# Kernel optimization log

Hardware: AMD Instinct MI355X
Metric: run time of the kernel (lower is better)

The kernel has to match this reference:

```python
import jax, jax.numpy as jnp
import numpy as np

P, V, D = 1024, 49408, 512


def setup_inputs() -> dict:
    key = jax.random.key(0)
    k1, k2 = jax.random.split(key)
    prompt_embs = jax.random.normal(k1, (P, D), dtype=jnp.float32)
    clip_embs = jax.random.normal(k2, (V, D), dtype=jnp.float32)
    return {"prompt_embs": prompt_embs, "clip_embs": clip_embs}


def reference(prompt_embs, clip_embs):
    # torch.cdist(p=2): Euclidean distance matrix [P, V].
    # ||a-b||^2 = ||a||^2 + ||b||^2 - 2 a.b ; sqrt is monotone so argmin of
    # the (clamped) squared distance matches argmin of the true distance.
    a2 = jnp.sum(prompt_embs * prompt_embs, axis=-1, keepdims=True)   # [P,1]
    b2 = jnp.sum(clip_embs * clip_embs, axis=-1)                      # [V]
    ab = jnp.einsum("pd,vd->pv", prompt_embs, clip_embs)              # [P,V]
    d2 = jnp.maximum(a2 + b2[None, :] - 2.0 * ab, 0.0)                # [P,V]
    prompt_ids = jnp.argmin(d2, axis=1)                               # [P]
    new_embs = clip_embs[prompt_ids]                                  # [P,D] gather
    return new_embs, prompt_ids
```

## Files before the change

kernel.cpp:

```cpp
#include <hip/hip_runtime.h>
#include <stdint.h>

#define NP 1024
#define NV 49408
#define ND 512
#define NTILE 48

typedef __attribute__((ext_vector_type(8))) __bf16 bf16x8;
typedef __attribute__((ext_vector_type(4))) float f32x4;
typedef __attribute__((ext_vector_type(4))) int i32x4;

__device__ inline unsigned long long pack_sv(float s, unsigned v) {
  unsigned u = __float_as_uint(s);
  u = (u & 0x80000000u) ? ~u : (u | 0x80000000u);
  return ((unsigned long long)u << 32) | (unsigned long long)v;
}

__global__ __launch_bounds__(256) void pack_a_k(const float* __restrict__ src,
                                                __bf16* __restrict__ dst) {
  int lane = threadIdx.x & 63;
  int row = blockIdx.x * 4 + (threadIdx.x >> 6);
  const float* r = src + (size_t)row * ND + lane * 8;
  float4 x0 = *(const float4*)r;
  float4 x1 = *(const float4*)(r + 4);
  float xs[8] = {x0.x, x0.y, x0.z, x0.w, x1.x, x1.y, x1.z, x1.w};
  bf16x8 hi, lo;
#pragma unroll
  for (int j = 0; j < 8; ++j) {
    float x = xs[j];
    __bf16 h = (__bf16)x;
    hi[j] = h;
    lo[j] = (__bf16)(x - (float)h);
  }
  const int mb = row >> 4, rr = row & 15;
  const int tHi = lane >> 2, g = lane & 3;
  size_t cHi = (((size_t)tHi * 64) + mb) * 64 + g * 16 + rr;
  size_t cLo = (((size_t)(tHi + 16) * 64) + mb) * 64 + g * 16 + rr;
  *(bf16x8*)(dst + cHi * 8) = hi;
  *(bf16x8*)(dst + cLo * 8) = lo;
}

__global__ __launch_bounds__(256) void pack_b_k(const float* __restrict__ src,
                                                __bf16* __restrict__ dst,
                                                float* __restrict__ sumsq) {
  int lane = threadIdx.x & 63;
  int row = blockIdx.x * 4 + (threadIdx.x >> 6);
  const float* r = src + (size_t)row * ND + lane * 8;
  float4 x0 = *(const float4*)r;
  float4 x1 = *(const float4*)(r + 4);
  float xs[8] = {x0.x, x0.y, x0.z, x0.w, x1.x, x1.y, x1.z, x1.w};
  bf16x8 hi, lo;
  float ss = 0.f;
#pragma unroll
  for (int j = 0; j < 8; ++j) {
    float x = xs[j];
    ss += x * x;
    __bf16 h = (__bf16)x;
    hi[j] = h;
    lo[j] = (__bf16)(x - (float)h);
  }
  __bf16* drow = dst + (size_t)row * 1024 + lane * 8;
  *(bf16x8*)drow = hi;
  *(bf16x8*)(drow + 512) = lo;
#pragma unroll
  for (int m = 1; m < 64; m <<= 1) ss += __shfl_xor(ss, m);
  if (lane == 0) sumsq[row] = ss;
}


__device__ __attribute__((always_inline)) static inline
void gll16(const char* src, char* dst) {
  __builtin_amdgcn_global_load_lds(
      (const __attribute__((address_space(1))) void*)src,
      (__attribute__((address_space(3))) void*)dst, 16, 0, 0);
}

__device__ __attribute__((always_inline)) static inline
bf16x8 lds_read(unsigned addr) {
  i32x4 d;
  asm volatile("ds_read_b128 %0, %1" : "=v"(d) : "v"(addr));
  return __builtin_bit_cast(bf16x8, d);
}

#define FENCE asm volatile("" ::: "memory")

__device__ __attribute__((always_inline)) static inline
int bByte(int t) {
  int tt = (t < NTILE) ? t : t - NTILE;
  return (tt & 15) * 64 + (tt >= 32 ? 1024 : 0);
}

template <int J>
__device__ __attribute__((always_inline)) static inline
void phase_op(f32x4 (&acc)[4][4], bf16x8 (&aE)[4], bf16x8 (&aO)[4],
              const char* Ab, const int (&voffA)[4],
              const char* srcBt, char* stB, unsigned bRead, int p) {
  constexpr int R0 = 2 * J, R1 = 2 * J + 1;
  constexpr int S0 = (2 * J + 4) % 6, S1 = (2 * J + 5) % 6;
  const int kB0 = bByte(2 * p + 4), kB1 = bByte(2 * p + 5);
  const int kAE = ((2 * p + 2) & 31) * 65536;
  const int kAO = ((2 * p + 3) & 31) * 65536;
  gll16(srcBt + kB0, stB + S0 * 8192);
  gll16(srcBt + kB0 + 131072, stB + S0 * 8192 + 4096);
  gll16(srcBt + kB1, stB + S1 * 8192);
  gll16(srcBt + kB1 + 131072, stB + S1 * 8192 + 4096);
  bf16x8 b0[4], b1[4];
#pragma unroll
  for (int n = 0; n < 4; ++n) b0[n] = lds_read(bRead + R0 * 8192 + n * 1024);
#pragma unroll
  for (int n = 0; n < 4; ++n) b1[n] = lds_read(bRead + R1 * 8192 + n * 1024);
  asm volatile("s_waitcnt vmcnt(8) lgkmcnt(4)" ::: "memory");
  __builtin_amdgcn_sched_barrier(0);
  __builtin_amdgcn_s_setprio(1);
#pragma unroll
  for (int m = 0; m < 4; ++m)
#pragma unroll
    for (int n = 0; n < 4; ++n)
      acc[m][n] = __builtin_amdgcn_mfma_f32_16x16x32_bf16(aE[m], b0[n], acc[m][n], 0, 0, 0);
  __builtin_amdgcn_s_setprio(0);
#pragma unroll
  for (int m = 0; m < 4; ++m)
    aE[m] = *(const bf16x8*)(Ab + voffA[m] + kAE);
  asm volatile("s_waitcnt vmcnt(8) lgkmcnt(0)" ::: "memory");
  __builtin_amdgcn_sched_barrier(0);
  __builtin_amdgcn_s_setprio(1);
#pragma unroll
  for (int m = 0; m < 4; ++m)
#pragma unroll
    for (int n = 0; n < 4; ++n)
      acc[m][n] = __builtin_amdgcn_mfma_f32_16x16x32_bf16(aO[m], b1[n], acc[m][n], 0, 0, 0);
  __builtin_amdgcn_s_setprio(0);
#pragma unroll
  for (int m = 0; m < 4; ++m)
    aO[m] = *(const bf16x8*)(Ab + voffA[m] + kAO);
  FENCE;
  __builtin_amdgcn_s_barrier();
  FENCE;
}

__global__ __launch_bounds__(256, 3) void gemm_argmin_k(const __bf16* __restrict__ A,
                                                        const __bf16* __restrict__ B,
                                                        const float* __restrict__ b2,
                                                        unsigned long long* __restrict__ best) {
  __shared__ __align__(16) char lds[49152];
  const int tid = threadIdx.x;
  const int lane = tid & 63;
  const int wid = tid >> 6;
  const int wm = wid >> 1;
  const int wn = wid & 1;

  const int d = blockIdx.x;
  const int o = (d & 7) * 386 + (d >> 3);
  const int bm = (o & 7) * 128;
  const int bn = (o >> 3) * 128;

  const int r = lane & 15, g = lane >> 4;
  const int rh = r >> 1;
  const unsigned lds0 =
      (unsigned)(uintptr_t)(const __attribute__((address_space(3))) char*)(const char*)lds;
  const unsigned bRead = lds0 + wn * 4096 + rh * 128 + (r & 1) * 64 + (((g + rh) & 3) << 4);

  const char* Ab = (const char*)A;
  int voffA[4];
#pragma unroll
  for (int m = 0; m < 4; ++m)
    voffA[m] = ((bm >> 4) + wm * 4 + m) * 1024 + lane * 16;

  const int srow = 2 * (tid >> 3) + ((tid >> 2) & 1);
  const int sc16 = ((tid & 3) - (tid >> 3)) & 3;
  const char* srcBt = (const char*)B + (size_t)(bn + srow) * 2048 + sc16 * 16;
  char* stB = (char*)lds + tid * 16;

  f32x4 acc[4][4] = {};
  bf16x8 aE[4], aO[4];

  gll16(srcBt + bByte(0), stB + 0);
  gll16(srcBt + bByte(0) + 131072, stB + 4096);
  gll16(srcBt + bByte(1), stB + 8192);
  gll16(srcBt + bByte(1) + 131072, stB + 8192 + 4096);
  gll16(srcBt + bByte(2), stB + 16384);
  gll16(srcBt + bByte(2) + 131072, stB + 16384 + 4096);
  gll16(srcBt + bByte(3), stB + 24576);
  gll16(srcBt + bByte(3) + 131072, stB + 24576 + 4096);
#pragma unroll
  for (int m = 0; m < 4; ++m)
    aE[m] = *(const bf16x8*)(Ab + voffA[m]);
#pragma unroll
  for (int m = 0; m < 4; ++m)
    aO[m] = *(const bf16x8*)(Ab + voffA[m] + 65536);
  asm volatile("s_waitcnt vmcnt(12)" ::: "memory");
  FENCE;
  __builtin_amdgcn_s_barrier();
  FENCE;

#pragma unroll 1
  for (int it = 0; it < 8; ++it) {
    const int p0 = 3 * it;
    phase_op<0>(acc, aE, aO, Ab, voffA, srcBt, stB, bRead, p0 + 0);
    phase_op<1>(acc, aE, aO, Ab, voffA, srcBt, stB, bRead, p0 + 1);
    phase_op<2>(acc, aE, aO, Ab, voffA, srcBt, stB, bRead, p0 + 2);
  }

  float bb[4];
#pragma unroll
  for (int n = 0; n < 4; ++n) bb[n] = b2[bn + wn * 64 + n * 16 + r];
#pragma unroll
  for (int m = 0; m < 4; ++m) {
#pragma unroll
    for (int reg = 0; reg < 4; ++reg) {
      unsigned long long pk = ~0ull;
#pragma unroll
      for (int n = 0; n < 4; ++n) {
        float s = bb[n] - 2.0f * acc[m][n][reg];
        unsigned long long cand = pack_sv(s, (unsigned)(bn + wn * 64 + n * 16 + r));
        pk = (cand < pk) ? cand : pk;
      }
#pragma unroll
      for (int msk = 1; msk < 16; msk <<= 1) {
        unsigned long long o2 = __shfl_xor(pk, msk);
        pk = (o2 < pk) ? o2 : pk;
      }
      if (r == 0) atomicMin(&best[bm + wm * 64 + m * 16 + g * 4 + reg], pk);
    }
  }
}

__global__ __launch_bounds__(256) void naive_argmin_k(const float* __restrict__ A,
                                                      const float* __restrict__ B,
                                                      unsigned long long* __restrict__ best) {
  __shared__ float arow[ND];
  int p = blockIdx.y;
  unsigned v = blockIdx.x * 256 + threadIdx.x;
  for (int i = threadIdx.x; i < ND; i += 256) arow[i] = A[(size_t)p * ND + i];
  __syncthreads();
  const float4* br = (const float4*)(B + (size_t)v * ND);
  float s = 0.f;
#pragma unroll 4
  for (int i = 0; i < ND / 4; ++i) {
    float4 b = br[i];
    const float4 a = *(const float4*)&arow[i * 4];
    float d0 = a.x - b.x, d1 = a.y - b.y, d2 = a.z - b.z, d3 = a.w - b.w;
    s += d0 * d0 + d1 * d1 + d2 * d2 + d3 * d3;
  }
  unsigned long long pk = pack_sv(s, v);
#pragma unroll
  for (int msk = 1; msk < 64; msk <<= 1) {
    unsigned long long o = __shfl_xor(pk, msk);
    pk = (o < pk) ? o : pk;
  }
  if ((threadIdx.x & 63) == 0) atomicMin(&best[p], pk);
}

__global__ __launch_bounds__(128) void gather_k(const unsigned long long* __restrict__ best,
                                                const float* __restrict__ clip,
                                                float* __restrict__ out) {
  int p = blockIdx.x;
  unsigned long long pk = best[p];
  unsigned v = (unsigned)(pk & 0xffffffffull);
  const float4* src = (const float4*)(clip + (size_t)v * ND);
  float4* dst = (float4*)(out + (size_t)p * ND);
  dst[threadIdx.x] = src[threadIdx.x];
  if (threadIdx.x == 0) out[(size_t)NP * ND + p] = (float)v;
}

extern "C" void kernel_launch(void* const* d_in, const int* in_sizes, int n_in,
                              void* d_out, int out_size, void* d_ws, size_t ws_size,
                              hipStream_t stream) {
  const float* prompt = (const float*)d_in[0];
  const float* clip = (const float*)d_in[1];
  float* out = (float*)d_out;

  size_t off = 0;
  unsigned long long* best = (unsigned long long*)d_ws;
  off += (size_t)NP * 8;
  float* b2 = (float*)((char*)d_ws + off);
  off += (size_t)NV * 4;
  off = (off + 255) & ~(size_t)255;
  __bf16* Ap = (__bf16*)((char*)d_ws + off);
  off += (size_t)NP * 1024 * 2;
  __bf16* Bp = (__bf16*)((char*)d_ws + off);
  off += (size_t)NV * 1024 * 2;
  const size_t need = off;

  if (ws_size >= need) {
    hipMemsetAsync(best, 0xFF, (size_t)NP * 8, stream);
    pack_a_k<<<NP / 4, 256, 0, stream>>>(prompt, Ap);
    pack_b_k<<<NV / 4, 256, 0, stream>>>(clip, Bp, b2);
    gemm_argmin_k<<<dim3(8 * 386), 256, 0, stream>>>(Ap, Bp, b2, best);
    gather_k<<<NP, 128, 0, stream>>>(best, clip, out);
  } else {
    hipMemsetAsync(best, 0xFF, (size_t)NP * 8, stream);
    dim3 grid(NV / 256, NP);
    naive_argmin_k<<<grid, 256, 0, stream>>>(prompt, clip, best);
    gather_k<<<NP, 128, 0, stream>>>(best, clip, out);
  }
}
```

Before: 213.2 us.

## Restructure K-loop schedule to reuse B tiles across two A halves

```diff
diff --git a/kernel.cpp b/kernel.cpp
--- a/kernel.cpp
+++ b/kernel.cpp
@@ -4,7 +4,6 @@
 #define NP 1024
 #define NV 49408
 #define ND 512
-#define NTILE 48
 
 typedef __attribute__((ext_vector_type(8))) __bf16 bf16x8;
 typedef __attribute__((ext_vector_type(4))) float f32x4;
@@ -84,32 +83,41 @@
 
 #define FENCE asm volatile("" ::: "memory")
 
-__device__ __attribute__((always_inline)) static inline
-int bByte(int t) {
-  int tt = (t < NTILE) ? t : t - NTILE;
-  return (tt & 15) * 64 + (tt >= 32 ? 1024 : 0);
-}
-
 template <int J>
 __device__ __attribute__((always_inline)) static inline
 void phase_op(f32x4 (&acc)[4][4], bf16x8 (&aE)[4], bf16x8 (&aO)[4],
               const char* Ab, const int (&voffA)[4],
-              const char* srcBt, char* stB, unsigned bRead, int p) {
-  constexpr int R0 = 2 * J, R1 = 2 * J + 1;
-  constexpr int S0 = (2 * J + 4) % 6, S1 = (2 * J + 5) % 6;
-  const int kB0 = bByte(2 * p + 4), kB1 = bByte(2 * p + 5);
-  const int kAE = ((2 * p + 2) & 31) * 65536;
-  const int kAO = ((2 * p + 3) & 31) * 65536;
-  gll16(srcBt + kB0, stB + S0 * 8192);
-  gll16(srcBt + kB0 + 131072, stB + S0 * 8192 + 4096);
-  gll16(srcBt + kB1, stB + S1 * 8192);
-  gll16(srcBt + kB1 + 131072, stB + S1 * 8192 + 4096);
+              const char* srcBt, char* stB, unsigned bRead) {
+  constexpr bool TK = (J >= 16);
+  constexpr int Q = J + 2, QA = J + 1;
+  constexpr int RB0 = TK ? (16 + 2 * (J - 16)) % 6 : (J % 6);
+  constexpr int RB1 = TK ? (17 + 2 * (J - 16)) % 6 : 0;
+  constexpr int DN = (Q <= 15) ? 1 : 2;
+  constexpr int SP0 = (Q <= 15) ? Q : (Q <= 23 ? 16 + 2 * (Q - 16) : (Q == 24 ? 0 : 2));
+  constexpr int SP1 = (Q <= 15) ? 0 : (Q <= 23 ? 17 + 2 * (Q - 16) : (Q == 24 ? 1 : 3));
+  constexpr int SR0 = (Q <= 15) ? (Q % 6) : ((16 + 2 * (Q - 16)) % 6);
+  constexpr int SR1 = (Q <= 15) ? 0 : ((17 + 2 * (Q - 16)) % 6);
+  constexpr int kB0 = (SP0 & 15) * 64 + (SP0 >= 16 ? 1024 : 0);
+  constexpr int kB1 = (SP1 & 15) * 64 + (SP1 >= 16 ? 1024 : 0);
+  constexpr int kAE = (QA <= 15 ? QA : (QA <= 23 ? 2 * (QA - 16) : 0)) * 65536;
+  constexpr int kAO = (QA <= 15 ? QA + 16 : (QA <= 23 ? 2 * (QA - 16) + 1 : 1)) * 65536;
+
+  gll16(srcBt + kB0, stB + SR0 * 8192);
+  gll16(srcBt + kB0 + 131072, stB + SR0 * 8192 + 4096);
+  if constexpr (DN == 2) {
+    gll16(srcBt + kB1, stB + SR1 * 8192);
+    gll16(srcBt + kB1 + 131072, stB + SR1 * 8192 + 4096);
+  }
   bf16x8 b0[4], b1[4];
 #pragma unroll
-  for (int n = 0; n < 4; ++n) b0[n] = lds_read(bRead + R0 * 8192 + n * 1024);
-#pragma unroll
-  for (int n = 0; n < 4; ++n) b1[n] = lds_read(bRead + R1 * 8192 + n * 1024);
-  asm volatile("s_waitcnt vmcnt(8) lgkmcnt(4)" ::: "memory");
+  for (int n = 0; n < 4; ++n) b0[n] = lds_read(bRead + RB0 * 8192 + n * 1024);
+  if constexpr (TK) {
+#pragma unroll
+    for (int n = 0; n < 4; ++n) b1[n] = lds_read(bRead + RB1 * 8192 + n * 1024);
+  }
+  if constexpr (TK) asm volatile("s_waitcnt vmcnt(8) lgkmcnt(4)" ::: "memory");
+  else if constexpr (DN == 2) asm volatile("s_waitcnt vmcnt(8) lgkmcnt(0)" ::: "memory");
+  else asm volatile("s_waitcnt vmcnt(6) lgkmcnt(0)" ::: "memory");
   __builtin_amdgcn_sched_barrier(0);
   __builtin_amdgcn_s_setprio(1);
 #pragma unroll
@@ -121,14 +129,16 @@
 #pragma unroll
   for (int m = 0; m < 4; ++m)
     aE[m] = *(const bf16x8*)(Ab + voffA[m] + kAE);
-  asm volatile("s_waitcnt vmcnt(8) lgkmcnt(0)" ::: "memory");
+  if constexpr (DN == 2) asm volatile("s_waitcnt vmcnt(8) lgkmcnt(0)" ::: "memory");
+  else asm volatile("s_waitcnt vmcnt(6) lgkmcnt(0)" ::: "memory");
   __builtin_amdgcn_sched_barrier(0);
   __builtin_amdgcn_s_setprio(1);
 #pragma unroll
   for (int m = 0; m < 4; ++m)
 #pragma unroll
     for (int n = 0; n < 4; ++n)
-      acc[m][n] = __builtin_amdgcn_mfma_f32_16x16x32_bf16(aO[m], b1[n], acc[m][n], 0, 0, 0);
+      acc[m][n] = __builtin_amdgcn_mfma_f32_16x16x32_bf16(aO[m], TK ? b1[n] : b0[n],
+                                                          acc[m][n], 0, 0, 0);
   __builtin_amdgcn_s_setprio(0);
 #pragma unroll
   for (int m = 0; m < 4; ++m)
@@ -174,32 +184,45 @@
   f32x4 acc[4][4] = {};
   bf16x8 aE[4], aO[4];
 
-  gll16(srcBt + bByte(0), stB + 0);
-  gll16(srcBt + bByte(0) + 131072, stB + 4096);
-  gll16(srcBt + bByte(1), stB + 8192);
-  gll16(srcBt + bByte(1) + 131072, stB + 8192 + 4096);
-  gll16(srcBt + bByte(2), stB + 16384);
-  gll16(srcBt + bByte(2) + 131072, stB + 16384 + 4096);
-  gll16(srcBt + bByte(3), stB + 24576);
-  gll16(srcBt + bByte(3) + 131072, stB + 24576 + 4096);
+  gll16(srcBt + 0, stB + 0);
+  gll16(srcBt + 0 + 131072, stB + 4096);
+  gll16(srcBt + 64, stB + 8192);
+  gll16(srcBt + 64 + 131072, stB + 8192 + 4096);
 #pragma unroll
   for (int m = 0; m < 4; ++m)
     aE[m] = *(const bf16x8*)(Ab + voffA[m]);
 #pragma unroll
   for (int m = 0; m < 4; ++m)
-    aO[m] = *(const bf16x8*)(Ab + voffA[m] + 65536);
-  asm volatile("s_waitcnt vmcnt(12)" ::: "memory");
+    aO[m] = *(const bf16x8*)(Ab + voffA[m] + 16 * 65536);
+  asm volatile("s_waitcnt vmcnt(10)" ::: "memory");
   FENCE;
   __builtin_amdgcn_s_barrier();
   FENCE;
 
-#pragma unroll 1
-  for (int it = 0; it < 8; ++it) {
-    const int p0 = 3 * it;
-    phase_op<0>(acc, aE, aO, Ab, voffA, srcBt, stB, bRead, p0 + 0);
-    phase_op<1>(acc, aE, aO, Ab, voffA, srcBt, stB, bRead, p0 + 1);
-    phase_op<2>(acc, aE, aO, Ab, voffA, srcBt, stB, bRead, p0 + 2);
-  }
+  phase_op<0>(acc, aE, aO, Ab, voffA, srcBt, stB, bRead);
+  phase_op<1>(acc, aE, aO, Ab, voffA, srcBt, stB, bRead);
+  phase_op<2>(acc, aE, aO, Ab, voffA, srcBt, stB, bRead);
+  phase_op<3>(acc, aE, aO, Ab, voffA, srcBt, stB, bRead);
+  phase_op<4>(acc, aE, aO, Ab, voffA, srcBt, stB, bRead);
+  phase_op<5>(acc, aE, aO, Ab, voffA, srcBt, stB, bRead);
+  phase_op<6>(acc, aE, aO, Ab, voffA, srcBt, stB, bRead);
+  phase_op<7>(acc, aE, aO, Ab, voffA, srcBt, stB, bRead);
+  phase_op<8>(acc, aE, aO, Ab, voffA, srcBt, stB, bRead);
+  phase_op<9>(acc, aE, aO, Ab, voffA, srcBt, stB, bRead);
+  phase_op<10>(acc, aE, aO, Ab, voffA, srcBt, stB, bRead);
+  phase_op<11>(acc, aE, aO, Ab, voffA, srcBt, stB, bRead);
+  phase_op<12>(acc, aE, aO, Ab, voffA, srcBt, stB, bRead);
+  phase_op<13>(acc, aE, aO, Ab, voffA, srcBt, stB, bRead);
+  phase_op<14>(acc, aE, aO, Ab, voffA, srcBt, stB, bRead);
+  phase_op<15>(acc, aE, aO, Ab, voffA, srcBt, stB, bRead);
+  phase_op<16>(acc, aE, aO, Ab, voffA, srcBt, stB, bRead);
+  phase_op<17>(acc, aE, aO, Ab, voffA, srcBt, stB, bRead);
+  phase_op<18>(acc, aE, aO, Ab, voffA, srcBt, stB, bRead);
+  phase_op<19>(acc, aE, aO, Ab, voffA, srcBt, stB, bRead);
+  phase_op<20>(acc, aE, aO, Ab, voffA, srcBt, stB, bRead);
+  phase_op<21>(acc, aE, aO, Ab, voffA, srcBt, stB, bRead);
+  phase_op<22>(acc, aE, aO, Ab, voffA, srcBt, stB, bRead);
+  phase_op<23>(acc, aE, aO, Ab, voffA, srcBt, stB, bRead);
 
   float bb[4];
 #pragma unroll
```

New measurement: 219.4 us. +2.9%, slower.
